# Kernel optimization log

Measured on AMD Instinct MI355X. Metric: run time of the kernel, lower is better.

The kernel has to match this reference:

```python
import jax, jax.numpy as jnp
import numpy as np

B, N, D, O, L = 16, 2000, 128, 64, 3  # batch, n_nodes, hidden_dim, output_dim, n_layers


def _init(key, shape, fan_in):
    return jax.random.normal(key, shape, jnp.float32) / np.sqrt(fan_in).astype(np.float32)


def setup_inputs() -> dict:
    key = jax.random.key(0)
    ks = jax.random.split(key, 8)
    return {
        "coords": jax.random.normal(ks[0], (B, N, 2), jnp.float32),
        "enc_w0": _init(ks[1], (2, D), 2),
        "enc_b0": jnp.zeros((D,), jnp.float32),
        "enc_w1": _init(ks[2], (D, D), D),
        "enc_b1": jnp.zeros((D,), jnp.float32),
        "gat_W": _init(ks[3], (L, D, D), D),      # per-layer GAT projection (no bias)
        "gat_a1": _init(ks[4], (L, D), 2 * D),    # first half of attention vector a
        "gat_a2": _init(ks[5], (L, D), 2 * D),    # second half of attention vector a
        "proj_w": _init(ks[6], (D, O), D),
        "proj_b": jnp.zeros((O,), jnp.float32),
    }


def _leaky(x):
    return jnp.where(x >= 0, x, 0.2 * x)  # LeakyReLU(0.2)


def reference(coords, enc_w0, enc_b0, enc_w1, enc_b1, gat_W, gat_a1, gat_a2, proj_w, proj_b):
    # node encoder: Linear -> ReLU -> Linear
    h = jax.nn.relu(coords @ enc_w0 + enc_b0) @ enc_w1 + enc_b1  # [B,N,D]
    n_layers = gat_W.shape[0]
    for l in range(n_layers):
        Wh = h @ gat_W[l]                      # [B,N,D]
        # additive GAT attention: e_ij = leakyrelu(a1.Wh_i + a2.Wh_j)
        # (equivalent to a([Wh_i || Wh_j]) without materializing N*N*2D tensor)
        e1 = Wh @ gat_a1[l]                    # [B,N]
        e2 = Wh @ gat_a2[l]                    # [B,N]
        e = _leaky(e1[:, :, None] + e2[:, None, :])  # [B,N,N]
        # adj is all-ones in forward() so the masked_fill is a no-op
        att = jax.nn.softmax(e, axis=-1)       # [B,N,N]; dropout is identity (eval)
        h = jax.nn.relu(att @ Wh)              # [B,N,D]
    return h @ proj_w + proj_b                 # [B,N,O]
```

## Files before the change

### kernel.cpp

```cpp
#include <hip/hip_runtime.h>
#include <hip/hip_bf16.h>

using bf16 = __hip_bfloat16;

#define BATCH 16
#define NNODE 2000
#define DIM   128
#define ODIM  64
#define NLAYER 3
#define BN    (BATCH*NNODE)
#define NP1   (NNODE+1)
#define CHK   125
#define CKS   16

#define OFF_COORDS 0
#define OFF_EW0    64000
#define OFF_EB0    64256
#define OFF_EW1    64384
#define OFF_EB1    80768
#define OFF_GW     80896
#define OFF_GA1    130048
#define OFF_GA2    130432
#define OFF_PW     130816
#define OFF_PB     139008
#define CVT_TOT    139072

#define PK_ENC     0
#define PK_GAT(l)  (32768 + (l)*32768)
#define PK_PROJ    131072
#define PK_TOT     147456

typedef __attribute__((ext_vector_type(8))) short bf16x8;
typedef __attribute__((ext_vector_type(4))) float f32x4;

__device__ __forceinline__ unsigned short f2bf(float f){
    union { float f; unsigned u; } x; x.f = f;
    unsigned r = (x.u + 0x7FFFu + ((x.u >> 16) & 1u)) >> 16;
    return (unsigned short)r;
}
__device__ __forceinline__ float bf2f(unsigned short h){
    union { unsigned u; float f; } x; x.u = ((unsigned)h) << 16;
    return x.f;
}

struct InPtrs { const void* p[10]; };

__global__ void convert_all_k(InPtrs in, float* __restrict__ dst, float* __restrict__ flag)
{
    __shared__ int scnt[256];
    const unsigned short* raw = (const unsigned short*)in.p[0];
    int t = threadIdx.x, c = 0;
    for (int k = t; k < 2048; k += 256){
        unsigned short u = raw[2*k];
        int e = (u >> 7) & 0xFF;
        if (e >= 100 && e <= 140) ++c;
    }
    scnt[t] = c;
    __syncthreads();
    for (int s = 128; s; s >>= 1){ if (t < s) scnt[t] += scnt[t+s]; __syncthreads(); }
    const bool isbf16 = (scnt[0] >= 1800);
    if (blockIdx.x == 0 && t == 0) flag[0] = isbf16 ? 1.0f : 0.0f;

    const int off[11] = {OFF_COORDS,OFF_EW0,OFF_EB0,OFF_EW1,OFF_EB1,
                         OFF_GW,OFF_GA1,OFF_GA2,OFF_PW,OFF_PB,CVT_TOT};
    int i = blockIdx.x*256 + t;
    if (i >= CVT_TOT) return;
    int seg = 0;
    #pragma unroll
    for (int s = 1; s < 10; ++s) if (i >= off[s]) seg = s;
    int li = i - off[seg];
    if (isbf16) dst[i] = __bfloat162float(((const bf16*)in.p[seg])[li]);
    else        dst[i] = ((const float*)in.p[seg])[li];
}

__global__ __launch_bounds__(256) void prep_k(const float* __restrict__ cvt,
                                              unsigned short* __restrict__ pk,
                                              float* __restrict__ wa)
{
    const int mi = blockIdx.x, t = threadIdx.x;
    const float* W; unsigned short* dst; int N;
    if (mi == 0)      { W = cvt + OFF_EW1;                    dst = pk + PK_ENC;      N = 128; }
    else if (mi <= 3) { W = cvt + OFF_GW + (mi-1)*DIM*DIM;    dst = pk + PK_GAT(mi-1);N = 128; }
    else              { W = cvt + OFF_PW;                     dst = pk + PK_PROJ;     N = 64;  }
    const int tot = 128*N;
    unsigned short* dh = dst;
    unsigned short* dl = dst + tot;
    for (int e = t; e < tot; e += 256){
        int col = e >> 7, k = e & 127;
        float v = W[k*N + col];
        unsigned short hb = f2bf(v);
        unsigned short lb = f2bf(v - bf2f(hb));
        dh[e] = hb;
        dl[e] = lb;
    }
    if (mi >= 1 && mi <= 3){
        const int l = mi - 1;
        const float* av = cvt + ((t < 128) ? OFF_GA1 : OFF_GA2) + l*DIM;
        const int r = t & 127;
        float s = 0.f;
        for (int c2 = 0; c2 < 128; ++c2) s = fmaf(W[r*128 + c2], av[c2], s);
        wa[l*256 + (t >> 7)*128 + r] = s;
    }
}


__global__ __launch_bounds__(256) void encmfma_k(const float* __restrict__ cvt,
    const unsigned short* __restrict__ pk, float* __restrict__ h)
{
    __shared__ unsigned short sAh[64*128], sAl[64*128];
    const int t = threadIdx.x, r0 = blockIdx.x*64;
    const int wv = t >> 6, l = t & 63, lc = l & 15, lk = l >> 4;
    const unsigned short* ph = pk;
    const unsigned short* pl = pk + 16384;
    bf16x8 bh[2][4], bl[2][4];
    #pragma unroll
    for (int cg = 0; cg < 2; ++cg){
        const int col = wv*32 + cg*16 + lc;
        #pragma unroll
        for (int kc = 0; kc < 4; ++kc){
            const int k0 = kc*32 + lk*8;
            bh[cg][kc] = *(const bf16x8*)&ph[col*128 + k0];
            bl[cg][kc] = *(const bf16x8*)&pl[col*128 + k0];
        }
    }
    const int row = t >> 2, g = t & 3;
    const float* coords = cvt + OFF_COORDS;
    const float* w0  = cvt + OFF_EW0;
    const float* b0v = cvt + OFF_EB0;
    const int node = r0 + row;
    const float c0 = coords[2*node], c1 = coords[2*node+1];
    char* shb = (char*)sAh; char* slb = (char*)sAl;
    const int swz = (row & 7) << 4;
    #pragma unroll
    for (int i = 0; i < 8; ++i){
        const int ch = g + i*4, k0 = ch*4;
        float4 wa0 = *(const float4*)&w0[k0];
        float4 wb0 = *(const float4*)&w0[DIM + k0];
        float4 bq  = *(const float4*)&b0v[k0];
        float4 v;
        v.x = fmaf(c0, wa0.x, fmaf(c1, wb0.x, bq.x)); v.x = v.x > 0.f ? v.x : 0.f;
        v.y = fmaf(c0, wa0.y, fmaf(c1, wb0.y, bq.y)); v.y = v.y > 0.f ? v.y : 0.f;
        v.z = fmaf(c0, wa0.z, fmaf(c1, wb0.z, bq.z)); v.z = v.z > 0.f ? v.z : 0.f;
        v.w = fmaf(c0, wa0.w, fmaf(c1, wb0.w, bq.w)); v.w = v.w > 0.f ? v.w : 0.f;
        ushort4 hq, lq;
        hq.x = f2bf(v.x); lq.x = f2bf(v.x - bf2f(hq.x));
        hq.y = f2bf(v.y); lq.y = f2bf(v.y - bf2f(hq.y));
        hq.z = f2bf(v.z); lq.z = f2bf(v.z - bf2f(hq.z));
        hq.w = f2bf(v.w); lq.w = f2bf(v.w - bf2f(hq.w));
        const int bo = (ch*8) ^ swz;
        *(ushort4*)(shb + row*256 + bo) = hq;
        *(ushort4*)(slb + row*256 + bo) = lq;
    }
    __syncthreads();
    f32x4 acc[4][2] = {};
    #pragma unroll
    for (int m = 0; m < 4; ++m){
        const int ar = m*16 + lc, asw = (ar & 7) << 4;
        #pragma unroll
        for (int kc = 0; kc < 4; ++kc){
            const int bo = (kc*64 + lk*16) ^ asw;
            bf16x8 ah = *(bf16x8*)(shb + ar*256 + bo);
            bf16x8 al = *(bf16x8*)(slb + ar*256 + bo);
            #pragma unroll
            for (int cg = 0; cg < 2; ++cg){
                acc[m][cg] = __builtin_amdgcn_mfma_f32_16x16x32_bf16(ah, bh[cg][kc], acc[m][cg], 0, 0, 0);
                acc[m][cg] = __builtin_amdgcn_mfma_f32_16x16x32_bf16(ah, bl[cg][kc], acc[m][cg], 0, 0, 0);
                acc[m][cg] = __builtin_amdgcn_mfma_f32_16x16x32_bf16(al, bh[cg][kc], acc[m][cg], 0, 0, 0);
            }
        }
    }
    const float* eb1 = cvt + OFF_EB1;
    #pragma unroll
    for (int m = 0; m < 4; ++m){
        const int rg = r0 + m*16 + lk*4;
        #pragma unroll
        for (int cg = 0; cg < 2; ++cg){
            const int col = wv*32 + cg*16 + lc;
            const float bb = eb1[col];
            #pragma unroll
            for (int j = 0; j < 4; ++j) h[(size_t)(rg+j)*DIM + col] = acc[m][cg][j] + bb;
        }
    }
}

__global__ __launch_bounds__(256) void gatmfma_k(const float* __restrict__ A,
    const unsigned short* __restrict__ pk, const float* __restrict__ wa,
    float* __restrict__ Wh, float* __restrict__ e1p, float* __restrict__ e2p)
{
    __shared__ unsigned short sAh[64*128], sAl[64*128];
    const int t = threadIdx.x, r0 = blockIdx.x*64;
    const int wv = t >> 6, l = t & 63, lc = l & 15, lk = l >> 4;
    const unsigned short* ph = pk;
    const unsigned short* pl = pk + 16384;
    bf16x8 bh[2][4], bl[2][4];
    #pragma unroll
    for (int cg = 0; cg < 2; ++cg){
        const int col = wv*32 + cg*16 + lc;
        #pragma unroll
        for (int kc = 0; kc < 4; ++kc){
            const int k0 = kc*32 + lk*8;
            bh[cg][kc] = *(const bf16x8*)&ph[col*128 + k0];
            bl[cg][kc] = *(const bf16x8*)&pl[col*128 + k0];
        }
    }
    const int row = t >> 2, g = t & 3;
    const float* Ar = A + (size_t)(r0 + row)*DIM;
    char* shb = (char*)sAh; char* slb = (char*)sAl;
    const int swz = (row & 7) << 4;
    float e1 = 0.f, e2 = 0.f;
    #pragma unroll
    for (int i = 0; i < 8; ++i){
        const int ch = g + i*4;
        float4 a  = *(const float4*)&Ar[ch*4];
        float4 u1 = *(const float4*)&wa[ch*4];
        float4 u2 = *(const float4*)&wa[128 + ch*4];
        e1 = fmaf(a.x,u1.x, fmaf(a.y,u1.y, fmaf(a.z,u1.z, fmaf(a.w,u1.w, e1))));
        e2 = fmaf(a.x,u2.x, fmaf(a.y,u2.y, fmaf(a.z,u2.z, fmaf(a.w,u2.w, e2))));
        ushort4 hq, lq;
        hq.x = f2bf(a.x); lq.x = f2bf(a.x - bf2f(hq.x));
        hq.y = f2bf(a.y); lq.y = f2bf(a.y - bf2f(hq.y));
        hq.z = f2bf(a.z); lq.z = f2bf(a.z - bf2f(hq.z));
        hq.w = f2bf(a.w); lq.w = f2bf(a.w - bf2f(hq.w));
        const int bo = (ch*8) ^ swz;
        *(ushort4*)(shb + row*256 + bo) = hq;
        *(ushort4*)(slb + row*256 + bo) = lq;
    }
    e1 += __shfl_xor(e1, 1); e1 += __shfl_xor(e1, 2);
    e2 += __shfl_xor(e2, 1); e2 += __shfl_xor(e2, 2);
    if (g == 0){ e1p[r0 + row] = e1; e2p[r0 + row] = e2; }
    __syncthreads();
    f32x4 acc[4][2] = {};
    #pragma unroll
    for (int m = 0; m < 4; ++m){
        const int ar = m*16 + lc, asw = (ar & 7) << 4;
        #pragma unroll
        for (int kc = 0; kc < 4; ++kc){
            const int bo = (kc*64 + lk*16) ^ asw;
            bf16x8 ah = *(bf16x8*)(shb + ar*256 + bo);
            bf16x8 al = *(bf16x8*)(slb + ar*256 + bo);
            #pragma unroll
            for (int cg = 0; cg < 2; ++cg){
                acc[m][cg] = __builtin_amdgcn_mfma_f32_16x16x32_bf16(ah, bh[cg][kc], acc[m][cg], 0, 0, 0);
                acc[m][cg] = __builtin_amdgcn_mfma_f32_16x16x32_bf16(ah, bl[cg][kc], acc[m][cg], 0, 0, 0);
                acc[m][cg] = __builtin_amdgcn_mfma_f32_16x16x32_bf16(al, bh[cg][kc], acc[m][cg], 0, 0, 0);
            }
        }
    }
    #pragma unroll
    for (int m = 0; m < 4; ++m){
        const int rg = r0 + m*16 + lk*4;
        #pragma unroll
        for (int cg = 0; cg < 2; ++cg){
            const int col = wv*32 + cg*16 + lc;
            #pragma unroll
            for (int j = 0; j < 4; ++j) Wh[(size_t)(rg+j)*DIM + col] = acc[m][cg][j];
        }
    }
}

__global__ __launch_bounds__(256) void projmfma_k(const float* __restrict__ A,
    const unsigned short* __restrict__ pk, const float* __restrict__ bias,
    void* __restrict__ outp, const float* __restrict__ flag)
{
    __shared__ unsigned short sAh[64*128], sAl[64*128];
    const int t = threadIdx.x, r0 = blockIdx.x*64;
    const int wv = t >> 6, l = t & 63, lc = l & 15, lk = l >> 4;
    const unsigned short* ph = pk;
    const unsigned short* pl = pk + 8192;
    bf16x8 bh[4], bl[4];
    const int col = wv*16 + lc;
    #pragma unroll
    for (int kc = 0; kc < 4; ++kc){
        const int k0 = kc*32 + lk*8;
        bh[kc] = *(const bf16x8*)&ph[col*128 + k0];
        bl[kc] = *(const bf16x8*)&pl[col*128 + k0];
    }
    const int row = t >> 2, g = t & 3;
    const float* Ar = A + (size_t)(r0 + row)*DIM;
    char* shb = (char*)sAh; char* slb = (char*)sAl;
    const int swz = (row & 7) << 4;
    #pragma unroll
    for (int i = 0; i < 8; ++i){
        const int ch = g + i*4;
        float4 a = *(const float4*)&Ar[ch*4];
        ushort4 hq, lq;
        hq.x = f2bf(a.x); lq.x = f2bf(a.x - bf2f(hq.x));
        hq.y = f2bf(a.y); lq.y = f2bf(a.y - bf2f(hq.y));
        hq.z = f2bf(a.z); lq.z = f2bf(a.z - bf2f(hq.z));
        hq.w = f2bf(a.w); lq.w = f2bf(a.w - bf2f(hq.w));
        const int bo = (ch*8) ^ swz;
        *(ushort4*)(shb + row*256 + bo) = hq;
        *(ushort4*)(slb + row*256 + bo) = lq;
    }
    __syncthreads();
    f32x4 acc[4] = {};
    #pragma unroll
    for (int m = 0; m < 4; ++m){
        const int ar = m*16 + lc, asw = (ar & 7) << 4;
        #pragma unroll
        for (int kc = 0; kc < 4; ++kc){
            const int bo = (kc*64 + lk*16) ^ asw;
            bf16x8 ah = *(bf16x8*)(shb + ar*256 + bo);
            bf16x8 al = *(bf16x8*)(slb + ar*256 + bo);
            acc[m] = __builtin_amdgcn_mfma_f32_16x16x32_bf16(ah, bh[kc], acc[m], 0, 0, 0);
            acc[m] = __builtin_amdgcn_mfma_f32_16x16x32_bf16(ah, bl[kc], acc[m], 0, 0, 0);
            acc[m] = __builtin_amdgcn_mfma_f32_16x16x32_bf16(al, bh[kc], acc[m], 0, 0, 0);
        }
    }
    const float bb = bias[col];
    const bool isbf = (flag[0] != 0.0f);
    #pragma unroll
    for (int m = 0; m < 4; ++m){
        const int rg = r0 + m*16 + lk*4;
        #pragma unroll
        for (int j = 0; j < 4; ++j){
            float v = acc[m][j] + bb;
            size_t p = (size_t)(rg+j)*ODIM + col;
            if (isbf) ((bf16*)outp)[p] = __float2bfloat16(v);
            else      ((float*)outp)[p] = v;
        }
    }
}

#define WAVE_FENCE() __asm__ volatile("" ::: "memory")
__global__ void sort_k(const float* __restrict__ e2p, float* __restrict__ e2s, int* __restrict__ sidx,
                       float* __restrict__ wp, float* __restrict__ wn, float* __restrict__ e2m)
{
    __shared__ float v[2048];
    __shared__ int  ix[2048];
    const int b = blockIdx.x, t = threadIdx.x;
    for (int i = t; i < 2048; i += 1024){
        v[i]  = (i < NNODE) ? e2p[b*NNODE + i] : 3.0e38f;
        ix[i] = i;
    }
    __syncthreads();

    #pragma unroll 1
    for (int size = 2; size <= 128; size <<= 1){
        #pragma unroll 1
        for (int stride = size >> 1; stride > 0; stride >>= 1){
            int i = 2*t - (t & (stride-1));
            int j = i + stride;
            bool asc = ((i & size) == 0);
            float vi = v[i], vj = v[j];
            bool sw = asc ? (vi > vj) : (vi < vj);
            if (sw){ v[i]=vj; v[j]=vi; int tm=ix[i]; ix[i]=ix[j]; ix[j]=tm; }
            WAVE_FENCE();
        }
    }
    __syncthreads();

    #pragma unroll 1
    for (int size = 256; size <= 2048; size <<= 1){
        #pragma unroll 1
        for (int stride = size >> 1; stride >= 128; stride >>= 1){
            int i = 2*t - (t & (stride-1));
            int j = i + stride;
            bool asc = ((i & size) == 0);
            float vi = v[i], vj = v[j];
            bool sw = asc ? (vi > vj) : (vi < vj);
            if (sw){ v[i]=vj; v[j]=vi; int tm=ix[i]; ix[i]=ix[j]; ix[j]=tm; }
            __syncthreads();
        }
        #pragma unroll 1
        for (int stride = 64; stride > 0; stride >>= 1){
            int i = 2*t - (t & (stride-1));
            int j = i + stride;
            bool asc = ((i & size) == 0);
            float vi = v[i], vj = v[j];
            bool sw = asc ? (vi > vj) : (vi < vj);
            if (sw){ v[i]=vj; v[j]=vi; int tm=ix[i]; ix[i]=ix[j]; ix[j]=tm; }
            WAVE_FENCE();
        }
        __syncthreads();
    }

    float mx = v[NNODE-1];
    for (int i = t; i < NNODE; i += 1024){
        float val = v[i];
        e2s [b*NNODE+i] = val;
        sidx[b*NNODE+i] = ix[i];
        wp  [b*NNODE+i] = __expf(val - mx);
        wn  [b*NNODE+i] = __expf(0.2f*(val - mx));
    }
    if (t == 0) e2m[b] = mx;
}

__global__ void passA_k(const float* __restrict__ Wh, const int* __restrict__ sidx,
    const float* __restrict__ wp, const float* __restrict__ wn,
    float* __restrict__ chunkP, float* __restrict__ chunkN,
    float* __restrict__ schunkP, float* __restrict__ schunkN)
{
    const int b = blockIdx.x / CHK, c = blockIdx.x % CHK, d = threadIdx.x;
    const int base = b*NNODE;
    float sp=0.f, sn=0.f, ssp=0.f, ssn=0.f;
    #pragma unroll 4
    for (int r = c*CKS; r < c*CKS + CKS; ++r){
        int j = sidx[base + r];
        float whv = Wh[((size_t)base + j)*DIM + d];
        float wpv = wp[base + r], wnv = wn[base + r];
        sp = fmaf(wpv, whv, sp);  sn = fmaf(wnv, whv, sn);
        ssp += wpv;  ssn += wnv;
    }
    const int idx = b*CHK + c;
    chunkP[idx*DIM + d] = sp;
    chunkN[idx*DIM + d] = sn;
    if (d == 0){ schunkP[idx] = ssp; schunkN[idx] = ssn; }
}

__global__ __launch_bounds__(256) void passB_k(
    const float* __restrict__ chunkP, const float* __restrict__ chunkN,
    const float* __restrict__ schunkP, const float* __restrict__ schunkN,
    float* __restrict__ offP, float* __restrict__ offN,
    float* __restrict__ soffP, float* __restrict__ soffN)
{
    const int b = blockIdx.x, tid = threadIdx.x;
    const bool doP = (blockIdx.y == 0);
    const float* chunk  = doP ? chunkP  : chunkN;
    const float* schunk = doP ? schunkP : schunkN;
    float* off  = doP ? offP  : offN;
    float* soff = doP ? soffP : soffN;

    if (tid < 128){
        const int d = tid;
        float acc = 0.f, v[25];
        #pragma unroll
        for (int t = 0; t < 5; ++t){
            const int c0 = doP ? (4-t)*25 : t*25;
            #pragma unroll
            for (int k = 0; k < 25; ++k) v[k] = chunk[(b*CHK + c0 + k)*DIM + d];
            if (doP){
                #pragma unroll
                for (int k = 24; k >= 0; --k){ off[(b*CHK + c0 + k)*DIM + d] = acc; acc += v[k]; }
            } else {
                #pragma unroll
                for (int k = 0; k < 25; ++k){ off[(b*CHK + c0 + k)*DIM + d] = acc; acc += v[k]; }
            }
        }
    } else if (tid == 128){
        float sacc = 0.f, sv[25];
        #pragma unroll
        for (int t = 0; t < 5; ++t){
            const int c0 = doP ? (4-t)*25 : t*25;
            #pragma unroll
            for (int k = 0; k < 25; ++k) sv[k] = schunk[b*CHK + c0 + k];
            if (doP){
                #pragma unroll
                for (int k = 24; k >= 0; --k){ soff[b*CHK + c0 + k] = sacc; sacc += sv[k]; }
            } else {
                #pragma unroll
                for (int k = 0; k < 25; ++k){ soff[b*CHK + c0 + k] = sacc; sacc += sv[k]; }
            }
        }
    }
}

__global__ void passC_k(const float* __restrict__ Wh, const int* __restrict__ sidx,
    const float* __restrict__ wp, const float* __restrict__ wn,
    const float* __restrict__ offP, const float* __restrict__ offN,
    const float* __restrict__ soffP, const float* __restrict__ soffN,
    float* __restrict__ Ppos, float* __restrict__ Pneg,
    float* __restrict__ pposs, float* __restrict__ pnegs)
{
    const int b = blockIdx.x / CHK, c = blockIdx.x % CHK, d = threadIdx.x;
    const int base = b*NNODE;
    const size_t pb = (size_t)b*NP1;
    const int idx = b*CHK + c;
    const int r0 = c*CKS, r1 = r0 + CKS;

    if (c == CHK-1){
        Ppos[(pb + NNODE)*DIM + d] = 0.f;
        if (d == 0) pposs[pb + NNODE] = 0.f;
    }
    float pr = offP[idx*DIM + d], spr = soffP[idx];
    for (int r = r1-1; r >= r0; --r){
        int j = sidx[base + r];
        float whv = Wh[((size_t)base + j)*DIM + d];
        float wpv = wp[base + r];
        pr  = fmaf(wpv, whv, pr);
        spr += wpv;
        Ppos[(pb + r)*DIM + d] = pr;
        if (d == 0) pposs[pb + r] = spr;
    }
    float nr = offN[idx*DIM + d], snr = soffN[idx];
    for (int r = r0; r < r1; ++r){
        int j = sidx[base + r];
        float whv = Wh[((size_t)base + j)*DIM + d];
        float wnv = wn[base + r];
        Pneg[(pb + r)*DIM + d] = nr;
        if (d == 0) pnegs[pb + r] = snr;
        nr  = fmaf(wnv, whv, nr);
        snr += wnv;
    }
    if (c == CHK-1){
        Pneg[(pb + NNODE)*DIM + d] = nr;
        if (d == 0) pnegs[pb + NNODE] = snr;
    }
}

__global__ __launch_bounds__(128) void out16_k(const float* __restrict__ e1p,
    const float* __restrict__ e2s, const float* __restrict__ e2m,
    const float* __restrict__ Ppos, const float* __restrict__ Pneg,
    const float* __restrict__ pposs, const float* __restrict__ pnegs, float* __restrict__ h)
{
    __shared__ int   slo[CKS];
    __shared__ float sps[CKS], sns[CKS];
    const int b = blockIdx.x / CHK, c = blockIdx.x % CHK, d = threadIdx.x;
    const int base = b*NNODE, r0 = c*CKS;
    const size_t pb = (size_t)b*NP1;

    if (d < CKS){
        int row = base + r0 + d;
        float e1v = e1p[row];
        float s = e1v + e2m[b];
        float m = (s >= 0.f) ? s : 0.2f*s;
        sps[d] = __expf(s - m);
        sns[d] = __expf(0.2f*s - m);
        const float* es = e2s + base;
        float tt = -e1v;
        int lo = 0, hi = NNODE;
        while (lo < hi){ int mid = (lo+hi) >> 1; if (es[mid] < tt) lo = mid+1; else hi = mid; }
        slo[d] = lo;
    }
    __syncthreads();
    #pragma unroll 4
    for (int k = 0; k < CKS; ++k){
        int row = base + r0 + k;
        size_t kb = pb + slo[k];
        float numer = sps[k]*Ppos[kb*DIM + d] + sns[k]*Pneg[kb*DIM + d];
        float Z     = sps[k]*pposs[kb]        + sns[k]*pnegs[kb];
        float q = numer / Z;
        h[(size_t)row*DIM + d] = (q > 0.f) ? q : ((q == q) ? 0.f : q);
    }
}

extern "C" void kernel_launch(void* const* d_in, const int* in_sizes, int n_in,
                              void* d_out, int out_size, void* d_ws, size_t ws_size,
                              hipStream_t stream)
{
    (void)in_sizes; (void)n_in; (void)out_size; (void)ws_size;

    float* f = (float*)d_ws;
    float* flag    = f;  f += 4;
    float* cvt     = f;  f += CVT_TOT;
    float* h       = f;  f += (size_t)BN*DIM;
    float* Wh      = f;  f += (size_t)BN*DIM;
    float* Ppos    = f;  f += (size_t)BATCH*NP1*DIM;
    float* Pneg    = f;  f += (size_t)BATCH*NP1*DIM;
    float* chunkP  = f;  f += BATCH*CHK*DIM;
    float* chunkN  = f;  f += BATCH*CHK*DIM;
    float* offP    = f;  f += BATCH*CHK*DIM;
    float* offN    = f;  f += BATCH*CHK*DIM;
    float* schunkP = f;  f += BATCH*CHK;
    float* schunkN = f;  f += BATCH*CHK;
    float* soffP   = f;  f += BATCH*CHK;
    float* soffN   = f;  f += BATCH*CHK;
    float* e1p     = f;  f += BN;
    float* e2p     = f;  f += BN;
    float* e2s     = f;  f += BN;
    float* wp      = f;  f += BN;
    float* wn      = f;  f += BN;
    float* pposs   = f;  f += BATCH*NP1;
    float* pnegs   = f;  f += BATCH*NP1;
    float* e2m     = f;  f += 16;
    int*   sidx    = (int*)f;
    unsigned short* pk = (unsigned short*)(sidx + BN);
    float* wa      = (float*)(pk + PK_TOT);

    InPtrs ip;
    for (int i = 0; i < 10; ++i) ip.p[i] = d_in[i];
    convert_all_k<<<(CVT_TOT+255)/256, 256, 0, stream>>>(ip, cvt, flag);

    prep_k<<<5, 256, 0, stream>>>(cvt, pk, wa);

    encmfma_k<<<BN/64, 256, 0, stream>>>(cvt, pk + PK_ENC, h);

    for (int l = 0; l < NLAYER; ++l){
        gatmfma_k<<<BN/64, 256, 0, stream>>>(h, pk + PK_GAT(l), wa + l*256, Wh, e1p, e2p);
        sort_k<<<BATCH, 1024, 0, stream>>>(e2p, e2s, sidx, wp, wn, e2m);
        passA_k<<<BATCH*CHK, DIM, 0, stream>>>(Wh, sidx, wp, wn, chunkP, chunkN, schunkP, schunkN);
        passB_k<<<dim3(BATCH, 2), 256, 0, stream>>>(chunkP, chunkN, schunkP, schunkN,
                                                    offP, offN, soffP, soffN);
        passC_k<<<BATCH*CHK, DIM, 0, stream>>>(Wh, sidx, wp, wn, offP, offN, soffP, soffN,
                                               Ppos, Pneg, pposs, pnegs);
        out16_k<<<BATCH*CHK, DIM, 0, stream>>>(e1p, e2s, e2m, Ppos, Pneg, pposs, pnegs, h);
    }

    projmfma_k<<<BN/64, 256, 0, stream>>>(h, pk + PK_PROJ, cvt + OFF_PB, d_out, flag);
}
```

Before: 310.4 us.

## Replace bitonic sort with parallel rank-by-counting across more blocks

The single-block-per-batch bitonic sort of e2 values is replaced by a rank kernel. Each of 8 blocks per batch loads all keys (value mapped to an ordered integer, packed with the index) into shared memory, and each thread counts how many keys are smaller to find its output position. This removes the many barrier-separated bitonic stages and spreads the work over 128 blocks instead of 16. In exchange it does O(N^2) comparisons from shared memory and computes the max redundantly in every block.

```diff
diff --git a/kernel.cpp b/kernel.cpp
--- a/kernel.cpp
+++ b/kernel.cpp
@@ -41,6 +41,10 @@
 __device__ __forceinline__ float bf2f(unsigned short h){
     union { unsigned u; float f; } x; x.u = ((unsigned)h) << 16;
     return x.f;
+}
+__device__ __forceinline__ unsigned ordu(float f){
+    union { float f; unsigned u; } x; x.f = f;
+    return (x.u & 0x80000000u) ? ~x.u : (x.u | 0x80000000u);
 }
 
 struct InPtrs { const void* p[10]; };
@@ -322,68 +326,43 @@
     }
 }
 
-#define WAVE_FENCE() __asm__ volatile("" ::: "memory")
-__global__ void sort_k(const float* __restrict__ e2p, float* __restrict__ e2s, int* __restrict__ sidx,
-                       float* __restrict__ wp, float* __restrict__ wn, float* __restrict__ e2m)
-{
-    __shared__ float v[2048];
-    __shared__ int  ix[2048];
-    const int b = blockIdx.x, t = threadIdx.x;
-    for (int i = t; i < 2048; i += 1024){
-        v[i]  = (i < NNODE) ? e2p[b*NNODE + i] : 3.0e38f;
-        ix[i] = i;
-    }
+__global__ __launch_bounds__(256) void rank_k(const float* __restrict__ e2p,
+    float* __restrict__ e2s, int* __restrict__ sidx,
+    float* __restrict__ wp, float* __restrict__ wn, float* __restrict__ e2m)
+{
+    __shared__ __align__(16) unsigned long long skey[2000];
+    __shared__ float smax[4];
+    const int b = blockIdx.x >> 3, blk = blockIdx.x & 7, t = threadIdx.x;
+    const int base = b*NNODE;
+    float pm = -3.0e38f;
+    for (int k = t; k < NNODE; k += 256){
+        float v = e2p[base + k];
+        pm = fmaxf(pm, v);
+        skey[k] = ((unsigned long long)ordu(v) << 32) | (unsigned)k;
+    }
+    #pragma unroll
+    for (int m = 32; m; m >>= 1) pm = fmaxf(pm, __shfl_xor(pm, m));
+    if ((t & 63) == 0) smax[t >> 6] = pm;
     __syncthreads();
-
-    #pragma unroll 1
-    for (int size = 2; size <= 128; size <<= 1){
-        #pragma unroll 1
-        for (int stride = size >> 1; stride > 0; stride >>= 1){
-            int i = 2*t - (t & (stride-1));
-            int j = i + stride;
-            bool asc = ((i & size) == 0);
-            float vi = v[i], vj = v[j];
-            bool sw = asc ? (vi > vj) : (vi < vj);
-            if (sw){ v[i]=vj; v[j]=vi; int tm=ix[i]; ix[i]=ix[j]; ix[j]=tm; }
-            WAVE_FENCE();
-        }
-    }
-    __syncthreads();
-
-    #pragma unroll 1
-    for (int size = 256; size <= 2048; size <<= 1){
-        #pragma unroll 1
-        for (int stride = size >> 1; stride >= 128; stride >>= 1){
-            int i = 2*t - (t & (stride-1));
-            int j = i + stride;
-            bool asc = ((i & size) == 0);
-            float vi = v[i], vj = v[j];
-            bool sw = asc ? (vi > vj) : (vi < vj);
-            if (sw){ v[i]=vj; v[j]=vi; int tm=ix[i]; ix[i]=ix[j]; ix[j]=tm; }
-            __syncthreads();
-        }
-        #pragma unroll 1
-        for (int stride = 64; stride > 0; stride >>= 1){
-            int i = 2*t - (t & (stride-1));
-            int j = i + stride;
-            bool asc = ((i & size) == 0);
-            float vi = v[i], vj = v[j];
-            bool sw = asc ? (vi > vj) : (vi < vj);
-            if (sw){ v[i]=vj; v[j]=vi; int tm=ix[i]; ix[i]=ix[j]; ix[j]=tm; }
-            WAVE_FENCE();
-        }
-        __syncthreads();
-    }
-
-    float mx = v[NNODE-1];
-    for (int i = t; i < NNODE; i += 1024){
-        float val = v[i];
-        e2s [b*NNODE+i] = val;
-        sidx[b*NNODE+i] = ix[i];
-        wp  [b*NNODE+i] = __expf(val - mx);
-        wn  [b*NNODE+i] = __expf(0.2f*(val - mx));
-    }
-    if (t == 0) e2m[b] = mx;
+    const float mx = fmaxf(fmaxf(smax[0], smax[1]), fmaxf(smax[2], smax[3]));
+    if (blk == 0 && t == 0) e2m[b] = mx;
+
+    const int i = blk*256 + t;
+    if (i >= NNODE) return;
+    const float vi = e2p[base + i];
+    const unsigned long long ki = ((unsigned long long)ordu(vi) << 32) | (unsigned)i;
+    unsigned r = 0;
+    const ulonglong2* sk2 = (const ulonglong2*)skey;
+    #pragma unroll 4
+    for (int j2 = 0; j2 < NNODE/2; ++j2){
+        ulonglong2 w = sk2[j2];
+        r += (w.x < ki);
+        r += (w.y < ki);
+    }
+    e2s [base + r] = vi;
+    sidx[base + r] = i;
+    wp  [base + r] = __expf(vi - mx);
+    wn  [base + r] = __expf(0.2f*(vi - mx));
 }
 
 __global__ void passA_k(const float* __restrict__ Wh, const int* __restrict__ sidx,
@@ -577,7 +556,7 @@
 
     for (int l = 0; l < NLAYER; ++l){
         gatmfma_k<<<BN/64, 256, 0, stream>>>(h, pk + PK_GAT(l), wa + l*256, Wh, e1p, e2p);
-        sort_k<<<BATCH, 1024, 0, stream>>>(e2p, e2s, sidx, wp, wn, e2m);
+        rank_k<<<BATCH*8, 256, 0, stream>>>(e2p, e2s, sidx, wp, wn, e2m);
         passA_k<<<BATCH*CHK, DIM, 0, stream>>>(Wh, sidx, wp, wn, chunkP, chunkN, schunkP, schunkN);
         passB_k<<<dim3(BATCH, 2), 256, 0, stream>>>(chunkP, chunkN, schunkP, schunkN,
                                                     offP, offN, soffP, soffN);
```

Measured after the change: 363.3 us. +17.0%, slower.

## Fold encoder second linear into first GAT projection and pack sort keys

Applied to the files above, without the earlier changes.

Precomputes the product of the encoder's second weight matrix with the layer-0 GAT projection, plus a fused bias and attention vectors. This lets one MFMA kernel go straight from coords to layer-0 Wh, e1 and e2, removing the separate encoder GEMM and its h write/read. Separately, the bitonic sort now sorts packed 64-bit (order-preserving key, index) values, so each swap moves one word instead of two arrays. The folded weights change the floating-point rounding order, and the 64-bit keys double the per-element LDS traffic width.

```diff
diff --git a/kernel.cpp b/kernel.cpp
--- a/kernel.cpp
+++ b/kernel.cpp
@@ -25,7 +25,6 @@
 #define OFF_PB     139008
 #define CVT_TOT    139072
 
-#define PK_ENC     0
 #define PK_GAT(l)  (32768 + (l)*32768)
 #define PK_PROJ    131072
 #define PK_TOT     147456
@@ -40,6 +39,15 @@
 }
 __device__ __forceinline__ float bf2f(unsigned short h){
     union { unsigned u; float f; } x; x.u = ((unsigned)h) << 16;
+    return x.f;
+}
+__device__ __forceinline__ unsigned ordu(float f){
+    union { float f; unsigned u; } x; x.f = f;
+    return (x.u & 0x80000000u) ? ~x.u : (x.u | 0x80000000u);
+}
+__device__ __forceinline__ float iordu(unsigned u){
+    union { unsigned u; float f; } x;
+    x.u = (u & 0x80000000u) ? (u ^ 0x80000000u) : ~u;
     return x.f;
 }
 
@@ -78,34 +86,75 @@
                                               float* __restrict__ wa)
 {
     const int mi = blockIdx.x, t = threadIdx.x;
-    const float* W; unsigned short* dst; int N;
-    if (mi == 0)      { W = cvt + OFF_EW1;                    dst = pk + PK_ENC;      N = 128; }
-    else if (mi <= 3) { W = cvt + OFF_GW + (mi-1)*DIM*DIM;    dst = pk + PK_GAT(mi-1);N = 128; }
-    else              { W = cvt + OFF_PW;                     dst = pk + PK_PROJ;     N = 64;  }
-    const int tot = 128*N;
-    unsigned short* dh = dst;
-    unsigned short* dl = dst + tot;
-    for (int e = t; e < tot; e += 256){
-        int col = e >> 7, k = e & 127;
-        float v = W[k*N + col];
-        unsigned short hb = f2bf(v);
-        unsigned short lb = f2bf(v - bf2f(hb));
-        dh[e] = hb;
-        dl[e] = lb;
-    }
-    if (mi >= 1 && mi <= 3){
-        const int l = mi - 1;
-        const float* av = cvt + ((t < 128) ? OFF_GA1 : OFF_GA2) + l*DIM;
-        const int r = t & 127;
-        float s = 0.f;
-        for (int c2 = 0; c2 < 128; ++c2) s = fmaf(W[r*128 + c2], av[c2], s);
-        wa[l*256 + (t >> 7)*128 + r] = s;
-    }
-}
-
-
-__global__ __launch_bounds__(256) void encmfma_k(const float* __restrict__ cvt,
-    const unsigned short* __restrict__ pk, float* __restrict__ h)
+    if (mi < 3){
+        const float* W; unsigned short* dst; int N;
+        if (mi == 0)      { W = cvt + OFF_GW + 1*DIM*DIM;  dst = pk + PK_GAT(1); N = 128; }
+        else if (mi == 1) { W = cvt + OFF_GW + 2*DIM*DIM;  dst = pk + PK_GAT(2); N = 128; }
+        else              { W = cvt + OFF_PW;              dst = pk + PK_PROJ;   N = 64;  }
+        const int tot = 128*N;
+        unsigned short* dh = dst;
+        unsigned short* dl = dst + tot;
+        for (int e = t; e < tot; e += 256){
+            int col = e >> 7, k = e & 127;
+            float v = W[k*N + col];
+            unsigned short hb = f2bf(v);
+            unsigned short lb = f2bf(v - bf2f(hb));
+            dh[e] = hb;
+            dl[e] = lb;
+        }
+    } else {
+        for (int idx = t; idx < 3*256; idx += 256){
+            const int l = idx >> 8, rem = idx & 255, half = rem >> 7, r = rem & 127;
+            const float* W  = cvt + OFF_GW + l*DIM*DIM;
+            const float* av = cvt + (half ? OFF_GA2 : OFF_GA1) + l*DIM;
+            float s = 0.f;
+            for (int c2 = 0; c2 < 128; ++c2) s = fmaf(W[r*128 + c2], av[c2], s);
+            wa[l*256 + half*128 + r] = s;
+        }
+    }
+}
+
+__global__ __launch_bounds__(128) void prep2_k(const float* __restrict__ cvt,
+    unsigned short* __restrict__ pk, const float* __restrict__ wa,
+    float* __restrict__ u12, float* __restrict__ bfuse, float* __restrict__ su)
+{
+    const int b = blockIdx.x, t = threadIdx.x;
+    const float* w1 = cvt + OFF_EW1;
+    const float* W0 = cvt + OFF_GW;
+    if (b < 128){
+        float acc = 0.f;
+        for (int d = 0; d < 128; ++d) acc = fmaf(w1[b*DIM + d], W0[d*DIM + t], acc);
+        unsigned short hb = f2bf(acc), lb = f2bf(acc - bf2f(hb));
+        unsigned short* dst = pk + PK_GAT(0);
+        dst[t*128 + b]         = hb;
+        dst[16384 + t*128 + b] = lb;
+    } else if (b == 128){
+        const float* b1 = cvt + OFF_EB1;
+        float acc = 0.f;
+        for (int d = 0; d < 128; ++d) acc = fmaf(b1[d], W0[d*DIM + t], acc);
+        bfuse[t] = acc;
+        if (t < 2){
+            float s = 0.f;
+            for (int d = 0; d < 128; ++d) s = fmaf(b1[d], wa[t*128 + d], s);
+            su[t] = s;
+        }
+    } else {
+        float a1 = 0.f, a2 = 0.f;
+        for (int d = 0; d < 128; ++d){
+            float w = w1[t*DIM + d];
+            a1 = fmaf(w, wa[d],       a1);
+            a2 = fmaf(w, wa[128 + d], a2);
+        }
+        u12[t]       = a1;
+        u12[128 + t] = a2;
+    }
+}
+
+
+__global__ __launch_bounds__(256) void gat0mfma_k(const float* __restrict__ cvt,
+    const unsigned short* __restrict__ pk, const float* __restrict__ u12,
+    const float* __restrict__ su, const float* __restrict__ bfuse,
+    float* __restrict__ Wh, float* __restrict__ e1p, float* __restrict__ e2p)
 {
     __shared__ unsigned short sAh[64*128], sAl[64*128];
     const int t = threadIdx.x, r0 = blockIdx.x*64;
@@ -131,6 +180,7 @@
     const float c0 = coords[2*node], c1 = coords[2*node+1];
     char* shb = (char*)sAh; char* slb = (char*)sAl;
     const int swz = (row & 7) << 4;
+    float e1 = 0.f, e2 = 0.f;
     #pragma unroll
     for (int i = 0; i < 8; ++i){
         const int ch = g + i*4, k0 = ch*4;
@@ -142,6 +192,10 @@
         v.y = fmaf(c0, wa0.y, fmaf(c1, wb0.y, bq.y)); v.y = v.y > 0.f ? v.y : 0.f;
         v.z = fmaf(c0, wa0.z, fmaf(c1, wb0.z, bq.z)); v.z = v.z > 0.f ? v.z : 0.f;
         v.w = fmaf(c0, wa0.w, fmaf(c1, wb0.w, bq.w)); v.w = v.w > 0.f ? v.w : 0.f;
+        float4 q1 = *(const float4*)&u12[k0];
+        float4 q2 = *(const float4*)&u12[128 + k0];
+        e1 = fmaf(v.x,q1.x, fmaf(v.y,q1.y, fmaf(v.z,q1.z, fmaf(v.w,q1.w, e1))));
+        e2 = fmaf(v.x,q2.x, fmaf(v.y,q2.y, fmaf(v.z,q2.z, fmaf(v.w,q2.w, e2))));
         ushort4 hq, lq;
         hq.x = f2bf(v.x); lq.x = f2bf(v.x - bf2f(hq.x));
         hq.y = f2bf(v.y); lq.y = f2bf(v.y - bf2f(hq.y));
@@ -151,6 +205,9 @@
         *(ushort4*)(shb + row*256 + bo) = hq;
         *(ushort4*)(slb + row*256 + bo) = lq;
     }
+    e1 += __shfl_xor(e1, 1); e1 += __shfl_xor(e1, 2);
+    e2 += __shfl_xor(e2, 1); e2 += __shfl_xor(e2, 2);
+    if (g == 0){ e1p[r0 + row] = e1 + su[0]; e2p[r0 + row] = e2 + su[1]; }
     __syncthreads();
     f32x4 acc[4][2] = {};
     #pragma unroll
@@ -169,16 +226,15 @@
             }
         }
     }
-    const float* eb1 = cvt + OFF_EB1;
     #pragma unroll
     for (int m = 0; m < 4; ++m){
         const int rg = r0 + m*16 + lk*4;
         #pragma unroll
         for (int cg = 0; cg < 2; ++cg){
             const int col = wv*32 + cg*16 + lc;
-            const float bb = eb1[col];
+            const float bb = bfuse[col];
             #pragma unroll
-            for (int j = 0; j < 4; ++j) h[(size_t)(rg+j)*DIM + col] = acc[m][cg][j] + bb;
+            for (int j = 0; j < 4; ++j) Wh[(size_t)(rg+j)*DIM + col] = acc[m][cg][j] + bb;
         }
     }
 }
@@ -326,13 +382,11 @@
 __global__ void sort_k(const float* __restrict__ e2p, float* __restrict__ e2s, int* __restrict__ sidx,
                        float* __restrict__ wp, float* __restrict__ wn, float* __restrict__ e2m)
 {
-    __shared__ float v[2048];
-    __shared__ int  ix[2048];
+    __shared__ unsigned long long kv[2048];
     const int b = blockIdx.x, t = threadIdx.x;
-    for (int i = t; i < 2048; i += 1024){
-        v[i]  = (i < NNODE) ? e2p[b*NNODE + i] : 3.0e38f;
-        ix[i] = i;
-    }
+    for (int i = t; i < 2048; i += 1024)
+        kv[i] = (i < NNODE) ? (((unsigned long long)ordu(e2p[b*NNODE + i]) << 32) | (unsigned)i)
+                            : 0xFFFFFFFFFFFFFFFFull;
     __syncthreads();
 
     #pragma unroll 1
@@ -342,9 +396,9 @@
             int i = 2*t - (t & (stride-1));
             int j = i + stride;
             bool asc = ((i & size) == 0);
-            float vi = v[i], vj = v[j];
-            bool sw = asc ? (vi > vj) : (vi < vj);
-            if (sw){ v[i]=vj; v[j]=vi; int tm=ix[i]; ix[i]=ix[j]; ix[j]=tm; }
+            unsigned long long ki = kv[i], kj = kv[j];
+            bool sw = asc ? (ki > kj) : (ki < kj);
+            if (sw){ kv[i] = kj; kv[j] = ki; }
             WAVE_FENCE();
         }
     }
@@ -357,9 +411,9 @@
             int i = 2*t - (t & (stride-1));
             int j = i + stride;
             bool asc = ((i & size) == 0);
-            float vi = v[i], vj = v[j];
-            bool sw = asc ? (vi > vj) : (vi < vj);
-            if (sw){ v[i]=vj; v[j]=vi; int tm=ix[i]; ix[i]=ix[j]; ix[j]=tm; }
+            unsigned long long ki = kv[i], kj = kv[j];
+            bool sw = asc ? (ki > kj) : (ki < kj);
+            if (sw){ kv[i] = kj; kv[j] = ki; }
             __syncthreads();
         }
         #pragma unroll 1
@@ -367,19 +421,20 @@
             int i = 2*t - (t & (stride-1));
             int j = i + stride;
             bool asc = ((i & size) == 0);
-            float vi = v[i], vj = v[j];
-            bool sw = asc ? (vi > vj) : (vi < vj);
-            if (sw){ v[i]=vj; v[j]=vi; int tm=ix[i]; ix[i]=ix[j]; ix[j]=tm; }
+            unsigned long long ki = kv[i], kj = kv[j];
+            bool sw = asc ? (ki > kj) : (ki < kj);
+            if (sw){ kv[i] = kj; kv[j] = ki; }
             WAVE_FENCE();
         }
         __syncthreads();
     }
 
-    float mx = v[NNODE-1];
+    const float mx = iordu((unsigned)(kv[NNODE-1] >> 32));
     for (int i = t; i < NNODE; i += 1024){
-        float val = v[i];
+        unsigned long long key = kv[i];
+        float val = iordu((unsigned)(key >> 32));
         e2s [b*NNODE+i] = val;
-        sidx[b*NNODE+i] = ix[i];
+        sidx[b*NNODE+i] = (int)(key & 0xFFFFFFFFull);
         wp  [b*NNODE+i] = __expf(val - mx);
         wn  [b*NNODE+i] = __expf(0.2f*(val - mx));
     }
@@ -566,17 +621,23 @@
     int*   sidx    = (int*)f;
     unsigned short* pk = (unsigned short*)(sidx + BN);
     float* wa      = (float*)(pk + PK_TOT);
+    float* u12     = wa + 768;
+    float* bfuse   = u12 + 256;
+    float* su      = bfuse + 128;
 
     InPtrs ip;
     for (int i = 0; i < 10; ++i) ip.p[i] = d_in[i];
     convert_all_k<<<(CVT_TOT+255)/256, 256, 0, stream>>>(ip, cvt, flag);
 
-    prep_k<<<5, 256, 0, stream>>>(cvt, pk, wa);
-
-    encmfma_k<<<BN/64, 256, 0, stream>>>(cvt, pk + PK_ENC, h);
+    prep_k<<<4, 256, 0, stream>>>(cvt, pk, wa);
+    prep2_k<<<130, 128, 0, stream>>>(cvt, pk, wa, u12, bfuse, su);
 
     for (int l = 0; l < NLAYER; ++l){
-        gatmfma_k<<<BN/64, 256, 0, stream>>>(h, pk + PK_GAT(l), wa + l*256, Wh, e1p, e2p);
+        if (l == 0)
+            gat0mfma_k<<<BN/64, 256, 0, stream>>>(cvt, pk + PK_GAT(0), u12, su, bfuse,
+                                                  Wh, e1p, e2p);
+        else
+            gatmfma_k<<<BN/64, 256, 0, stream>>>(h, pk + PK_GAT(l), wa + l*256, Wh, e1p, e2p);
         sort_k<<<BATCH, 1024, 0, stream>>>(e2p, e2s, sidx, wp, wn, e2m);
         passA_k<<<BATCH*CHK, DIM, 0, stream>>>(Wh, sidx, wp, wn, chunkP, chunkN, schunkP, schunkN);
         passB_k<<<dim3(BATCH, 2), 256, 0, stream>>>(chunkP, chunkN, schunkP, schunkN,
```

Result: faster. 301.9 us (-2.8%).
